# Optimization experiments

Measured on AMD Instinct MI355X. Metric: run time of the kernel, lower is better.

## Reference

```python
import jax, jax.numpy as jnp
import numpy as np

B, S, D, UNITS = 8, 2048, 1024, 1024

def setup_inputs() -> dict:
    key = jax.random.key(0)
    k1, k2, k3, k4 = jax.random.split(key, 4)
    scale = 1.0 / np.sqrt(D)
    return {
        "inputs": jax.random.normal(k1, (B, S, D), dtype=jnp.float32),
        "Wq": jax.random.normal(k2, (D, UNITS), dtype=jnp.float32) * scale,
        "Wk": jax.random.normal(k3, (D, UNITS), dtype=jnp.float32) * scale,
        "Wv": jax.random.normal(k4, (D, UNITS), dtype=jnp.float32) * scale,
    }

def reference(inputs, Wq, Wk, Wv):
    # QKV projections (bias-free Dense): [B,S,D] @ [D,U] -> [B,S,U]
    q = jnp.einsum("bsd,du->bsu", inputs, Wq)
    k = jnp.einsum("bsd,du->bsu", inputs, Wk)
    v = jnp.einsum("bsd,du->bsu", inputs, Wv)
    # scaled dot-product scores [B,S,S]
    scores = jnp.einsum("bqu,bku->bqk", q, k) / jnp.sqrt(jnp.float32(UNITS))
    attn = jax.nn.softmax(scores, axis=-1)
    # weighted sum of values [B,S,U]
    return jnp.einsum("bqk,bku->bqu", attn, v)
```

## Files before the change

### kernel.cpp

```cpp
#include <hip/hip_runtime.h>


typedef _Float16 half8  __attribute__((ext_vector_type(8)));
typedef _Float16 half4v __attribute__((ext_vector_type(4)));
typedef _Float16 half2v __attribute__((ext_vector_type(2)));
typedef float    floatx4 __attribute__((ext_vector_type(4)));

__device__ __forceinline__ void stage_ht(const _Float16* __restrict__ src, int ld,
                                         _Float16* __restrict__ dst, int wave, int lane) {
#pragma unroll
    for (int i = 0; i < 2; ++i) {
        int q = wave * 2 + i;
        int c = q * 64 + lane;
        int row = c >> 3, c8 = c & 7;
        int cg = c8 ^ (row & 7);
        __builtin_amdgcn_global_load_lds(
            (const __attribute__((address_space(1))) unsigned int*)(src + (size_t)row * ld + cg * 8),
            (__attribute__((address_space(3))) unsigned int*)(dst + q * 512),
            16, 0, 0);
    }
}

__device__ __forceinline__ float sum8h(half8 a) {
    union { half8 v; half2v h2[4]; } u; u.v = a;
    half2v s0 = u.h2[0] + u.h2[1];
    half2v s1 = u.h2[2] + u.h2[3];
    half2v s  = s0 + s1;
    return (float)s[0] + (float)s[1];
}

#define SA_(T, h) stage_ht(A + (size_t)((h) * 128) * lda + (size_t)(T) * 64, lda, \
                           ShA + (((T) & 1) * 2 + (h)) * 8192, wave, lane)
#define SB_(T, h) stage_ht(B + (size_t)((h) * 128) * ldb + (size_t)(T) * 64, ldb, \
                           ShB + (((T) & 1) * 2 + (h)) * 8192, wave, lane)

#define LOADA(aq, i0)                                                        \
    _Pragma("unroll")                                                        \
    for (int ii = 0; ii < 2; ++ii) {                                         \
        int rr = ((i0) + ii) * 16 + l15;                                     \
        _Pragma("unroll")                                                    \
        for (int kk = 0; kk < 2; ++kk) {                                     \
            int cg = (kk * 4 + q4) ^ (rr & 7);                               \
            aq[ii][kk] = *(const half8*)(As + rr * 64 + cg * 8);             \
            if (RSUM) rsum[(i0) + ii] += sum8h(aq[ii][kk]);                  \
        }                                                                    \
    }

#define MFMAQ(aq, i0)                                                        \
    asm volatile("s_waitcnt lgkmcnt(0)" ::: "memory");                       \
    __builtin_amdgcn_s_setprio(1);                                           \
    _Pragma("unroll")                                                        \
    for (int kk = 0; kk < 2; ++kk)                                           \
        _Pragma("unroll")                                                    \
        for (int ii = 0; ii < 2; ++ii)                                       \
            _Pragma("unroll")                                                \
            for (int j = 0; j < 4; ++j)                                      \
                acc[(i0) + ii][j] = __builtin_amdgcn_mfma_f32_16x16x32_f16(  \
                    aq[ii][kk], b[j][kk], acc[(i0) + ii][j], 0, 0, 0);       \
    __builtin_amdgcn_s_setprio(0);

#define BARF() do { __builtin_amdgcn_s_barrier(); asm volatile("" ::: "memory"); } while (0)

template<bool RSUM>
__device__ __forceinline__ void gemm8p(const _Float16* __restrict__ A, int lda,
                                       const _Float16* __restrict__ B, int ldb,
                                       int K, _Float16* __restrict__ ShA,
                                       _Float16* __restrict__ ShB,
                                       int wave, int lane,
                                       floatx4 (&acc)[8][4], float (&rsum)[8]) {
    const int wm = wave >> 2, wn = wave & 3;
    const int l15 = lane & 15, q4 = lane >> 4;
    const int NT = K >> 6;

    SB_(0, 0); SB_(0, 1); SA_(0, 1); SA_(0, 0);
    if (NT > 1) { SB_(1, 0); SB_(1, 1); SA_(1, 1); }

    for (int t = 0; t < NT; ++t) {
        const _Float16* As = ShA + (t & 1) * 16384 + wm * 8192;
        const _Float16* Bs = ShB + (t & 1) * 16384 + (wn >> 1) * 8192;
        const int rb = (wn & 1) * 64;
        half8 b[4][2];
        half8 a0[2][2], a1[2][2], a2[2][2], a3[2][2];

        if (t + 1 < NT) SA_(t + 1, 0);
        if (t == NT - 1) asm volatile("s_waitcnt vmcnt(0)" ::: "memory");
        else             asm volatile("s_waitcnt vmcnt(8)" ::: "memory");
        BARF();
#pragma unroll
        for (int j = 0; j < 4; ++j) {
            int rr = rb + j * 16 + l15;
#pragma unroll
            for (int kk = 0; kk < 2; ++kk) {
                int cg = (kk * 4 + q4) ^ (rr & 7);
                b[j][kk] = *(const half8*)(Bs + rr * 64 + cg * 8);
            }
        }
        LOADA(a0, 0);
        MFMAQ(a0, 0);
        BARF();

        LOADA(a1, 2);
        if (t + 2 < NT) SB_(t + 2, 0);
        BARF();
        MFMAQ(a1, 2);
        BARF();

        LOADA(a2, 4);
        LOADA(a3, 6);
        if (t + 2 < NT) SB_(t + 2, 1);
        BARF();
        MFMAQ(a2, 4);
        BARF();

        if (t + 2 < NT) SA_(t + 2, 1);
        BARF();
        MFMAQ(a3, 6);
        BARF();
    }
}

__global__ void cast_x(const float* __restrict__ X, _Float16* __restrict__ Xh) {
    size_t i = ((size_t)blockIdx.x * 256 + threadIdx.x) * 8;
    float4 v0 = *(const float4*)(X + i);
    float4 v1 = *(const float4*)(X + i + 4);
    half8 hh;
    hh[0] = (_Float16)v0.x; hh[1] = (_Float16)v0.y; hh[2] = (_Float16)v0.z; hh[3] = (_Float16)v0.w;
    hh[4] = (_Float16)v1.x; hh[5] = (_Float16)v1.y; hh[6] = (_Float16)v1.z; hh[7] = (_Float16)v1.w;
    *(half8*)(Xh + i) = hh;
}

__global__ void prep_weights(const float* __restrict__ Wq, const float* __restrict__ Wk,
                             const float* __restrict__ Wv, _Float16* __restrict__ WbT) {
    int g = blockIdx.z;
    const float* W = (g == 0) ? Wq : (g == 1) ? Wk : Wv;
    __shared__ float tile[32][33];
    int u0 = blockIdx.x * 32, d0 = blockIdx.y * 32;
    int tx = threadIdx.x & 31, ty = threadIdx.x >> 5;
#pragma unroll
    for (int i = 0; i < 32; i += 8)
        tile[ty + i][tx] = W[(size_t)(d0 + ty + i) * 1024 + (u0 + tx)];
    __syncthreads();
#pragma unroll
    for (int i = 0; i < 32; i += 8)
        WbT[(size_t)g * 1024 * 1024 + (size_t)(u0 + ty + i) * 1024 + (d0 + tx)] =
            (_Float16)tile[tx][ty + i];
}

__global__ __launch_bounds__(512, 2)
void qkv_gemm(const _Float16* __restrict__ Xh, const _Float16* __restrict__ WbT,
              _Float16* __restrict__ Qh, _Float16* __restrict__ Kh,
              _Float16* __restrict__ Vt) {
    __shared__ __align__(16) _Float16 ShA[32768];
    __shared__ __align__(16) _Float16 ShB[32768];
    int t = threadIdx.x;
    int lane = t & 63, wave = t >> 6;
    int wm = wave >> 2, wn = wave & 3;
    int l15 = lane & 15, q4 = lane >> 4;
    int which = blockIdx.x >> 2;
    int u0 = (blockIdx.x & 3) * 256;
    int m0 = blockIdx.y * 256;
    const _Float16* A = Xh + (size_t)m0 * 1024;
    const _Float16* B = WbT + (size_t)which * 1024 * 1024 + (size_t)u0 * 1024;
    floatx4 acc[8][4] = {};
    float rsum[8] = {};
    gemm8p<false>(A, 1024, B, 1024, 1024, ShA, ShB, wave, lane, acc, rsum);

    int bz = m0 >> 11;
    int sbase = (m0 & 2047) + wm * 128;
    if (which < 2) {
        _Float16* db = (which ? Kh : Qh) + (size_t)bz * 2048 * 1024;
#pragma unroll
        for (int i = 0; i < 8; ++i)
#pragma unroll
            for (int j = 0; j < 4; ++j)
#pragma unroll
                for (int r = 0; r < 4; ++r) {
                    int s = sbase + i * 16 + q4 * 4 + r;
                    int u = u0 + wn * 64 + j * 16 + l15;
                    db[(size_t)s * 1024 + u] = (_Float16)acc[i][j][r];
                }
    } else {
        _Float16* vb = Vt + (size_t)bz * 1024 * 2048;
#pragma unroll
        for (int i = 0; i < 8; ++i)
#pragma unroll
            for (int j = 0; j < 4; ++j) {
                int s = sbase + i * 16 + q4 * 4;
                int u = u0 + wn * 64 + j * 16 + l15;
                half4v pk;
#pragma unroll
                for (int r = 0; r < 4; ++r) pk[r] = (_Float16)acc[i][j][r];
                *(half4v*)(vb + (size_t)u * 2048 + s) = pk;
            }
    }
}

__global__ __launch_bounds__(512, 2)
void scores_gemm(const _Float16* __restrict__ Qh, const _Float16* __restrict__ Kh,
                 _Float16* __restrict__ P) {
    __shared__ __align__(16) _Float16 ShA[32768];
    __shared__ __align__(16) _Float16 ShB[32768];
    int t = threadIdx.x;
    int lane = t & 63, wave = t >> 6;
    int wm = wave >> 2, wn = wave & 3;
    int l15 = lane & 15, q4 = lane >> 4;
    int m0 = blockIdx.y * 256, n0 = blockIdx.x * 256;
    int batch = blockIdx.z;
    const _Float16* A = Qh + (size_t)batch * 2048 * 1024 + (size_t)m0 * 1024;
    const _Float16* B = Kh + (size_t)batch * 2048 * 1024 + (size_t)n0 * 1024;
    floatx4 acc[8][4] = {};
    float rsum[8] = {};
    gemm8p<false>(A, 1024, B, 1024, 1024, ShA, ShB, wave, lane, acc, rsum);

    _Float16* Pb = P + (size_t)batch * 2048 * 2048;
#pragma unroll
    for (int i = 0; i < 8; ++i)
#pragma unroll
        for (int j = 0; j < 4; ++j)
#pragma unroll
            for (int r = 0; r < 4; ++r) {
                int m = m0 + wm * 128 + i * 16 + q4 * 4 + r;
                int n = n0 + wn * 64 + j * 16 + l15;
                Pb[(size_t)m * 2048 + n] = (_Float16)__expf(acc[i][j][r] * 0.03125f);
            }
}

__global__ __launch_bounds__(512, 2)
void pv_gemm(const _Float16* __restrict__ P, const _Float16* __restrict__ Vt,
             float* __restrict__ out) {
    __shared__ __align__(16) _Float16 ShA[32768];
    __shared__ __align__(16) _Float16 ShB[32768];
    int t = threadIdx.x;
    int lane = t & 63, wave = t >> 6;
    int wm = wave >> 2, wn = wave & 3;
    int l15 = lane & 15, q4 = lane >> 4;
    int m0 = blockIdx.y * 256, n0 = blockIdx.x * 256;
    int batch = blockIdx.z;
    const _Float16* A = P + (size_t)batch * 2048 * 2048 + (size_t)m0 * 2048;
    const _Float16* B = Vt + (size_t)batch * 1024 * 2048 + (size_t)n0 * 2048;
    floatx4 acc[8][4] = {};
    float rsum[8] = {};
    gemm8p<true>(A, 2048, B, 2048, 2048, ShA, ShB, wave, lane, acc, rsum);

    float rsumf[8];
#pragma unroll
    for (int i = 0; i < 8; ++i) {
        float v = rsum[i] + __shfl_xor(rsum[i], 16);
        rsumf[i] = v + __shfl_xor(v, 32);
    }
    float* ob = out + (size_t)batch * 2048 * 1024;
#pragma unroll
    for (int i = 0; i < 8; ++i)
#pragma unroll
        for (int r = 0; r < 4; ++r) {
            int rloc = q4 * 4 + r;
            float inv = 1.0f / __shfl(rsumf[i], rloc);
            int m = m0 + wm * 128 + i * 16 + rloc;
#pragma unroll
            for (int j = 0; j < 4; ++j) {
                int n = n0 + wn * 64 + j * 16 + l15;
                ob[(size_t)m * 1024 + n] = acc[i][j][r] * inv;
            }
        }
}

extern "C" void kernel_launch(void* const* d_in, const int* in_sizes, int n_in,
                              void* d_out, int out_size, void* d_ws, size_t ws_size,
                              hipStream_t stream) {
    const float* X  = (const float*)d_in[0];
    const float* Wq = (const float*)d_in[1];
    const float* Wk = (const float*)d_in[2];
    const float* Wv = (const float*)d_in[3];
    float* out = (float*)d_out;

    char* ws = (char*)d_ws;
    size_t off = 0;
    _Float16* Xh  = (_Float16*)(ws + off); off += (size_t)8 * 2048 * 1024 * 2;
    _Float16* WbT = (_Float16*)(ws + off); off += (size_t)3 * 1024 * 1024 * 2;
    _Float16* Qh  = (_Float16*)(ws + off); off += (size_t)8 * 2048 * 1024 * 2;
    _Float16* Kh  = (_Float16*)(ws + off); off += (size_t)8 * 2048 * 1024 * 2;
    _Float16* Vt  = (_Float16*)(ws + off); off += (size_t)8 * 1024 * 2048 * 2;
    _Float16* P   = (_Float16*)(ws + off); off += (size_t)8 * 2048 * 2048 * 2;

    cast_x      <<<dim3(8192, 1, 1), 256, 0, stream>>>(X, Xh);
    prep_weights<<<dim3(32, 32, 3), 256, 0, stream>>>(Wq, Wk, Wv, WbT);
    qkv_gemm    <<<dim3(12, 64, 1), 512, 0, stream>>>(Xh, WbT, Qh, Kh, Vt);
    scores_gemm <<<dim3(8, 8, 8),   512, 0, stream>>>(Qh, Kh, P);
    pv_gemm     <<<dim3(4, 8, 8),   512, 0, stream>>>(P, Vt, out);
}
```

Before: 452.7 us.

## Restructure GEMM main loop into k-split phases with reordered LDS staging

Rewrites the inner GEMM loop so that each 64-wide k tile is processed in four phases. Each phase reads four A fragments and four B fragments for one k half and issues 16 MFMAs, which cuts the live fragment registers from 24 half8 to 8. Global-to-LDS prefetch is rescheduled: A for the next tile is staged in two halves during the current tile, and B for tile t+2 is issued near the end. The vmcnt wait and barrier move to the end of the iteration. A sched_barrier is added before each MFMA block to pin instruction order. The aim is to lower register pressure and overlap loads better. The trade-off is that B fragments are now re-read from LDS per k half, with extra waits and barriers.

```diff
diff --git a/kernel.cpp b/kernel.cpp
--- a/kernel.cpp
+++ b/kernel.cpp
@@ -29,37 +29,49 @@
     return (float)s[0] + (float)s[1];
 }
 
+#define BARF() do { __builtin_amdgcn_s_barrier(); asm volatile("" ::: "memory"); } while (0)
+
 #define SA_(T, h) stage_ht(A + (size_t)((h) * 128) * lda + (size_t)(T) * 64, lda, \
                            ShA + (((T) & 1) * 2 + (h)) * 8192, wave, lane)
 #define SB_(T, h) stage_ht(B + (size_t)((h) * 128) * ldb + (size_t)(T) * 64, ldb, \
                            ShB + (((T) & 1) * 2 + (h)) * 8192, wave, lane)
 
-#define LOADA(aq, i0)                                                        \
-    _Pragma("unroll")                                                        \
-    for (int ii = 0; ii < 2; ++ii) {                                         \
-        int rr = ((i0) + ii) * 16 + l15;                                     \
-        _Pragma("unroll")                                                    \
-        for (int kk = 0; kk < 2; ++kk) {                                     \
-            int cg = (kk * 4 + q4) ^ (rr & 7);                               \
-            aq[ii][kk] = *(const half8*)(As + rr * 64 + cg * 8);             \
-            if (RSUM) rsum[(i0) + ii] += sum8h(aq[ii][kk]);                  \
-        }                                                                    \
-    }
-
-#define MFMAQ(aq, i0)                                                        \
-    asm volatile("s_waitcnt lgkmcnt(0)" ::: "memory");                       \
-    __builtin_amdgcn_s_setprio(1);                                           \
-    _Pragma("unroll")                                                        \
-    for (int kk = 0; kk < 2; ++kk)                                           \
-        _Pragma("unroll")                                                    \
-        for (int ii = 0; ii < 2; ++ii)                                       \
-            _Pragma("unroll")                                                \
-            for (int j = 0; j < 4; ++j)                                      \
-                acc[(i0) + ii][j] = __builtin_amdgcn_mfma_f32_16x16x32_f16(  \
-                    aq[ii][kk], b[j][kk], acc[(i0) + ii][j], 0, 0, 0);       \
+__device__ __forceinline__ void read_b(const _Float16* __restrict__ Bs, int rb,
+                                       int l15, int q4, int kk, half8 (&bf)[4]) {
+#pragma unroll
+    for (int j = 0; j < 4; ++j) {
+        int rr = rb + j * 16 + l15;
+        int cg = (kk * 4 + q4) ^ (rr & 7);
+        bf[j] = *(const half8*)(Bs + rr * 64 + cg * 8);
+    }
+}
+
+template<bool RSUM>
+__device__ __forceinline__ void read_a(const _Float16* __restrict__ As, int i0,
+                                       int l15, int q4, int kk, half8 (&af)[4],
+                                       float* rsum) {
+#pragma unroll
+    for (int ii = 0; ii < 4; ++ii) {
+        int rr = (i0 + ii) * 16 + l15;
+        int cg = (kk * 4 + q4) ^ (rr & 7);
+        af[ii] = *(const half8*)(As + rr * 64 + cg * 8);
+        if (RSUM) rsum[i0 + ii] += sum8h(af[ii]);
+    }
+}
+
+__device__ __forceinline__ void mfma16(const half8 (&af)[4], const half8 (&bf)[4],
+                                       int i0, floatx4 (&acc)[8][4]) {
+    asm volatile("s_waitcnt lgkmcnt(0)" ::: "memory");
+    __builtin_amdgcn_sched_barrier(0);
+    __builtin_amdgcn_s_setprio(1);
+#pragma unroll
+    for (int ii = 0; ii < 4; ++ii)
+#pragma unroll
+        for (int j = 0; j < 4; ++j)
+            acc[i0 + ii][j] = __builtin_amdgcn_mfma_f32_16x16x32_f16(
+                af[ii], bf[j], acc[i0 + ii][j], 0, 0, 0);
     __builtin_amdgcn_s_setprio(0);
-
-#define BARF() do { __builtin_amdgcn_s_barrier(); asm volatile("" ::: "memory"); } while (0)
+}
 
 template<bool RSUM>
 __device__ __forceinline__ void gemm8p(const _Float16* __restrict__ A, int lda,
@@ -72,49 +84,44 @@
     const int l15 = lane & 15, q4 = lane >> 4;
     const int NT = K >> 6;
 
-    SB_(0, 0); SB_(0, 1); SA_(0, 1); SA_(0, 0);
-    if (NT > 1) { SB_(1, 0); SB_(1, 1); SA_(1, 1); }
+    SB_(0, 0); SB_(0, 1); SA_(0, 0); SA_(0, 1);
+    SB_(1, 0); SB_(1, 1);
+    asm volatile("s_waitcnt vmcnt(4)" ::: "memory");
+    BARF();
 
     for (int t = 0; t < NT; ++t) {
         const _Float16* As = ShA + (t & 1) * 16384 + wm * 8192;
         const _Float16* Bs = ShB + (t & 1) * 16384 + (wn >> 1) * 8192;
         const int rb = (wn & 1) * 64;
-        half8 b[4][2];
-        half8 a0[2][2], a1[2][2], a2[2][2], a3[2][2];
-
+        half8 bf[4], af[4];
+
+        read_b(Bs, rb, l15, q4, 0, bf);
+        read_a<RSUM>(As, 0, l15, q4, 0, af, rsum);
         if (t + 1 < NT) SA_(t + 1, 0);
-        if (t == NT - 1) asm volatile("s_waitcnt vmcnt(0)" ::: "memory");
-        else             asm volatile("s_waitcnt vmcnt(8)" ::: "memory");
-        BARF();
-#pragma unroll
-        for (int j = 0; j < 4; ++j) {
-            int rr = rb + j * 16 + l15;
-#pragma unroll
-            for (int kk = 0; kk < 2; ++kk) {
-                int cg = (kk * 4 + q4) ^ (rr & 7);
-                b[j][kk] = *(const half8*)(Bs + rr * 64 + cg * 8);
-            }
+        BARF();
+        mfma16(af, bf, 0, acc);
+        BARF();
+
+        read_a<RSUM>(As, 4, l15, q4, 0, af, rsum);
+        if (t + 1 < NT) SA_(t + 1, 1);
+        BARF();
+        mfma16(af, bf, 4, acc);
+        BARF();
+
+        read_b(Bs, rb, l15, q4, 1, bf);
+        read_a<RSUM>(As, 0, l15, q4, 1, af, rsum);
+        BARF();
+        mfma16(af, bf, 0, acc);
+        BARF();
+
+        read_a<RSUM>(As, 4, l15, q4, 1, af, rsum);
+        if (t + 2 < NT) { SB_(t + 2, 0); SB_(t + 2, 1); }
+        BARF();
+        mfma16(af, bf, 4, acc);
+        if (t + 1 < NT) {
+            if (t + 2 < NT) asm volatile("s_waitcnt vmcnt(4)" ::: "memory");
+            else            asm volatile("s_waitcnt vmcnt(0)" ::: "memory");
         }
-        LOADA(a0, 0);
-        MFMAQ(a0, 0);
-        BARF();
-
-        LOADA(a1, 2);
-        if (t + 2 < NT) SB_(t + 2, 0);
-        BARF();
-        MFMAQ(a1, 2);
-        BARF();
-
-        LOADA(a2, 4);
-        LOADA(a3, 6);
-        if (t + 2 < NT) SB_(t + 2, 1);
-        BARF();
-        MFMAQ(a2, 4);
-        BARF();
-
-        if (t + 2 < NT) SA_(t + 2, 1);
-        BARF();
-        MFMAQ(a3, 6);
         BARF();
     }
 }
```

After: 390.4 us. 13.8% less time.
